# Kernel tuning notes

Hardware: AMD Instinct MI355X
Metric: run time of the kernel (lower is better)

Reference implementation:

```python
import jax, jax.numpy as jnp
import numpy as np
from jax import lax

V, E, Q, D = 100000, 300, 64, 4096
K = 5
NEG_SLOPE = 0.01


def setup_inputs() -> dict:
    key = jax.random.key(0)
    ks = jax.random.split(key, 16)
    return {
        "question": jax.random.randint(ks[0], (Q,), 0, V),
        "doc1": jax.random.randint(ks[1], (D,), 0, V),
        "doc2": jax.random.randint(ks[2], (D,), 0, V),
        "doc1_sim": jax.random.uniform(ks[3], (D, Q), dtype=jnp.float32),
        "doc2_sim": jax.random.uniform(ks[4], (D, Q), dtype=jnp.float32),
        "gaf": jax.random.normal(ks[5], (4,), dtype=jnp.float32),
        "baf": jax.random.normal(ks[6], (4,), dtype=jnp.float32),
        "emb": jax.random.normal(ks[7], (V, E), dtype=jnp.float32) * 0.1,
        "idf": jax.random.uniform(ks[8], (V, 1), dtype=jnp.float32) * 10.0,
        "conv_w": jax.random.normal(ks[9], (E, E, 3), dtype=jnp.float32) * (1.0 / np.sqrt(3 * E)),
        "conv_b": jax.random.normal(ks[10], (E,), dtype=jnp.float32) * 0.01,
        "qw_w": jax.random.normal(ks[11], (1, E + 1), dtype=jnp.float32) * (1.0 / np.sqrt(E + 1)),
        "qw_b": jax.random.normal(ks[12], (1,), dtype=jnp.float32) * 0.01,
        "lin1_w": jax.random.normal(ks[13], (8, 6), dtype=jnp.float32) * (1.0 / np.sqrt(6)),
        "lin2_w": jax.random.normal(ks[14], (1, 8), dtype=jnp.float32) * (1.0 / np.sqrt(8)),
        "out_w": jax.random.normal(ks[15], (1, 5), dtype=jnp.float32) * (1.0 / np.sqrt(5)),
    }


def _leaky(x):
    return jnp.where(x >= 0, x, NEG_SLOPE * x)


def _conv_residual(x, w, b):
    # x: [L, E]. Torch Conv1d(E,E,3,padding=2) followed by slice [1:L+1] is a
    # centered SAME conv; activation applied before the residual add.
    y = lax.conv_general_dilated(x.T[None], w, (1,), [(1, 1)],
                                 dimension_numbers=("NCW", "OIW", "NCW"))
    y = y[0] + b[:, None]            # [E, L]
    return _leaky(y).T + x           # [L, E]


def _cosine(A, B):
    # A: [Q, E], B: [L, E] -> [Q, L]
    num = A @ B.T
    den = jnp.linalg.norm(A, axis=-1)[:, None] * jnp.linalg.norm(B, axis=-1)[None, :]
    return num / den


def _kmax_pool(sim):
    # sim: [Q, L] -> [Q, 2] = (max, mean of top-K)
    top = lax.top_k(sim, K)[0]       # descending [Q, K]
    return jnp.stack([top[:, 0], jnp.mean(top, axis=-1)], axis=-1)


def _get_output(pooled_list, q_weights, lin1_w, lin2_w):
    temp = jnp.concatenate(pooled_list, axis=-1)     # [Q, 6]
    lo = _leaky(temp @ lin1_w.T) @ lin2_w.T          # [Q, 1]
    lo = lo[:, 0] * q_weights
    return jnp.sum(lo) / lo.shape[0]


def reference(question, doc1, doc2, doc1_sim, doc2_sim, gaf, baf,
              emb, idf, conv_w, conv_b, qw_w, qw_b, lin1_w, lin2_w, out_w):
    q_emb = emb[question]            # [Q, E]
    d1_emb = emb[doc1]               # [D, E]
    d2_emb = emb[doc2]

    sim_ins_d1 = _cosine(q_emb, d1_emb)
    sim_ins_d2 = _cosine(q_emb, d2_emb)

    q_conv = _conv_residual(q_emb, conv_w, conv_b)
    d1_conv = _conv_residual(d1_emb, conv_w, conv_b)
    d2_conv = _conv_residual(d2_emb, conv_w, conv_b)

    sim_sen_d1 = _cosine(q_conv, d1_conv)
    sim_sen_d2 = _cosine(q_conv, d2_conv)

    sim_oh_d1 = doc1_sim.T           # [Q, D]
    sim_oh_d2 = doc2_sim.T

    p_oh_d1, p_ins_d1, p_sen_d1 = _kmax_pool(sim_oh_d1), _kmax_pool(sim_ins_d1), _kmax_pool(sim_sen_d1)
    p_oh_d2, p_ins_d2, p_sen_d2 = _kmax_pool(sim_oh_d2), _kmax_pool(sim_ins_d2), _kmax_pool(sim_sen_d2)

    q_idfs = idf[question]           # [Q, 1]
    qw = jnp.concatenate([q_conv, q_idfs], axis=-1) @ qw_w.T + qw_b  # [Q, 1]
    q_weights = jax.nn.softmax(qw[:, 0], axis=-1)

    doc1_emit = _get_output([p_oh_d1, p_ins_d1, p_sen_d1], q_weights, lin1_w, lin2_w)
    doc2_emit = _get_output([p_oh_d2, p_ins_d2, p_sen_d2], q_weights, lin1_w, lin2_w)

    good_feats = jnp.concatenate([gaf, doc1_emit[None]])  # [5]
    bad_feats = jnp.concatenate([baf, doc2_emit[None]])
    good_out = out_w @ good_feats                          # [1]
    bad_out = out_w @ bad_feats

    loss1 = jnp.mean(jnp.maximum(0.0, -(good_out - bad_out) + 1.0))
    return (loss1, good_out, bad_out, loss1, loss1)
```

## Files before the change

### kernel.cpp

```cpp
#include <hip/hip_runtime.h>
#include <math.h>

#define EE 300
#define KP 320
#define LDSW 328
#define QQ 64
#define DD 4096
#define NEG 0.01f

typedef __attribute__((ext_vector_type(8))) short short8;
typedef __attribute__((ext_vector_type(4))) float f32x4;
typedef unsigned short ushort_t;

__device__ inline ushort_t f2bf(float f) {
  unsigned u = __builtin_bit_cast(unsigned, f);
  u += 0x7fff + ((u >> 16) & 1);
  return (ushort_t)(u >> 16);
}
__device__ inline float bf2f(ushort_t h) {
  return __builtin_bit_cast(float, (unsigned)h << 16);
}

#define GATHER_ROWS (66 + 4098 + 4098)
#define GATHER_BLOCKS ((GATHER_ROWS + 3) / 4)
#define WT_BLOCKS 143
#define TR_BLOCKS 128
#define ZERO_BLOCKS 9
#define PREP_BLOCKS (GATHER_BLOCKS + WT_BLOCKS + TR_BLOCKS + ZERO_BLOCKS)

__global__ __launch_bounds__(256) void prep(
    const float* __restrict__ emb, const int* __restrict__ question,
    const int* __restrict__ doc1, const int* __restrict__ doc2,
    const float* __restrict__ conv_w,
    const float* __restrict__ doc1_sim, const float* __restrict__ doc2_sim,
    ushort_t* __restrict__ qbe, ushort_t* __restrict__ d1be, ushort_t* __restrict__ d2be,
    ushort_t* __restrict__ qbc, ushort_t* __restrict__ d1bc, ushort_t* __restrict__ d2bc,
    ushort_t* __restrict__ wt2,
    float* __restrict__ ohT1, float* __restrict__ ohT2,
    float* __restrict__ nq2, float* __restrict__ nd12, float* __restrict__ nd22,
    float* __restrict__ acc_zero_base) {
  __shared__ float tilebuf[64][65];
  int b = blockIdx.x;
  int tid = threadIdx.x;
  if (b < GATHER_BLOCKS) {
    int w = tid >> 6, lane = tid & 63;
    int g = b * 4 + w;
    int t, row;
    if (g < 66)             { t = 0; row = g; }
    else if (g < 66 + 4098) { t = 1; row = g - 66; }
    else if (g < GATHER_ROWS) { t = 2; row = g - 66 - 4098; }
    else return;
    const int* idx = t == 0 ? question : (t == 1 ? doc1 : doc2);
    int L = t == 0 ? QQ : DD;
    ushort_t* be = t == 0 ? qbe : (t == 1 ? d1be : d2be);
    ushort_t* bc = t == 0 ? qbc : (t == 1 ? d1bc : d2bc);
    float* nrm2 = t == 0 ? nq2 : (t == 1 ? nd12 : nd22);
    if (row == 0 || row == L + 1) {
      for (int i = lane; i < KP; i += 64) be[(size_t)row * KP + i] = 0;
      return;
    }
    int r = row - 1;
    const float* src = emb + (size_t)idx[r] * EE;
    float ss = 0.f;
    for (int i = lane; i < EE; i += 64) {
      float v = src[i];
      be[(size_t)row * KP + i] = f2bf(v);
      ss += v * v;
    }
    for (int i = EE + lane; i < KP; i += 64) {
      be[(size_t)row * KP + i] = 0;
      bc[(size_t)r * KP + i] = 0;
    }
    #pragma unroll
    for (int o = 32; o; o >>= 1) ss += __shfl_xor(ss, o);
    if (lane == 0) nrm2[r] = ss;
  } else if (b < GATHER_BLOCKS + WT_BLOCKS) {
    int f = (b - GATHER_BLOCKS) * 4 + (tid >> 6);
    if (f >= 570) return;
    int lane = tid & 63;
    int ks = f % 10, n = (f / 10) % 19, tap = f / 190;
    int o = n * 16 + (lane & 15);
    int kbase = ks * 32 + (lane >> 4) * 8;
    ushort_t* dst = wt2 + (size_t)f * 512 + lane * 8;
    #pragma unroll
    for (int e = 0; e < 8; ++e) {
      int k = kbase + e;
      float v = (o < EE && k < EE) ? conv_w[((size_t)o * EE + k) * 3 + tap] : 0.f;
      dst[e] = f2bf(v);
    }
  } else if (b < GATHER_BLOCKS + WT_BLOCKS + TR_BLOCKS) {
    int idx = b - (GATHER_BLOCKS + WT_BLOCKS);
    int srcsel = idx >> 6, tile = idx & 63;
    const float* in = srcsel ? doc2_sim : doc1_sim;
    float* outT = srcsel ? ohT2 : ohT1;
    int c = tid & 63, rq = tid >> 6;
    #pragma unroll 4
    for (int i = 0; i < 16; ++i) {
      int r = i * 4 + rq;
      tilebuf[r][c] = in[(size_t)(tile * 64 + r) * QQ + c];
    }
    __syncthreads();
    #pragma unroll 4
    for (int i = 0; i < 16; ++i) {
      int q = i * 4 + rq;
      outT[(size_t)q * DD + tile * 64 + c] = tilebuf[c][q];
    }
  } else {
    int i0 = (b - (GATHER_BLOCKS + WT_BLOCKS + TR_BLOCKS)) * 1024 + tid;
    #pragma unroll
    for (int j = 0; j < 4; ++j) {
      int i = i0 + j * 256;
      if (i < 8320) acc_zero_base[i] = 0.f;
    }
  }
}

__global__ __launch_bounds__(256) void conv_mfma(
    const ushort_t* __restrict__ wt2, const float* __restrict__ bias,
    const float* __restrict__ qw_w,
    const ushort_t* __restrict__ qbe, const ushort_t* __restrict__ d1be,
    const ushort_t* __restrict__ d2be,
    ushort_t* __restrict__ qbc, ushort_t* __restrict__ d1bc,
    ushort_t* __restrict__ d2bc,
    float* __restrict__ nqc2, float* __restrict__ nd1c2, float* __restrict__ nd2c2,
    float* __restrict__ qwacc) {
  __shared__ ushort_t lds[34 * LDSW];
  int bx = blockIdx.x;
  int t, m0, yh;
  if (bx < 4) { t = 0; m0 = (bx >> 1) * 32; yh = bx & 1; }
  else {
    int i = bx - 4;
    t = 1 + (i >> 8);
    int j = i & 255;
    m0 = (j >> 1) * 32; yh = j & 1;
  }
  const ushort_t* be = t == 0 ? qbe : (t == 1 ? d1be : d2be);
  ushort_t* bc = t == 0 ? qbc : (t == 1 ? d1bc : d2bc);
  float* nc2 = t == 0 ? nqc2 : (t == 1 ? nd1c2 : nd2c2);
  int tid = threadIdx.x;
  for (int s = tid; s < 34 * 40; s += 256) {
    int row = s / 40, col = s - row * 40;
    *(short8*)(&lds[row * LDSW + col * 8]) =
        *(const short8*)(be + (size_t)(m0 + row) * KP + col * 8);
  }
  __syncthreads();
  int w = tid >> 6, lane = tid & 63, mrow = lane & 15, g = lane >> 4;
  int nstart, ncnt;
  if (yh == 0) { nstart = (w < 2) ? 3 * w : 2 * w + 2; ncnt = (w < 2) ? 3 : 2; }
  else         { nstart = (w == 0) ? 10 : 2 * w + 11;  ncnt = (w == 0) ? 3 : 2; }
  f32x4 acc[3][2];
  #pragma unroll
  for (int j = 0; j < 3; ++j)
    #pragma unroll
    for (int h = 0; h < 2; ++h) acc[j][h] = (f32x4){0.f, 0.f, 0.f, 0.f};

  for (int tap = 0; tap < 3; ++tap) {
    const ushort_t* alo = &lds[(mrow + tap) * LDSW + g * 8];
    #pragma unroll
    for (int ks = 0; ks < 10; ++ks) {
      short8 a0 = *(const short8*)(alo + ks * 32);
      short8 a1 = *(const short8*)(alo + 16 * LDSW + ks * 32);
      #pragma unroll
      for (int j = 0; j < 3; ++j) {
        if (j < ncnt) {
          short8 bfr = *(const short8*)(wt2 +
              (size_t)((tap * 19 + nstart + j) * 10 + ks) * 512 + lane * 8);
          acc[j][0] = __builtin_amdgcn_mfma_f32_16x16x32_bf16(a0, bfr, acc[j][0], 0, 0, 0);
          acc[j][1] = __builtin_amdgcn_mfma_f32_16x16x32_bf16(a1, bfr, acc[j][1], 0, 0, 0);
        }
      }
    }
  }
  float ss[2][4] = {{0.f,0.f,0.f,0.f},{0.f,0.f,0.f,0.f}};
  float yq[2][4] = {{0.f,0.f,0.f,0.f},{0.f,0.f,0.f,0.f}};
  #pragma unroll
  for (int j = 0; j < 3; ++j) {
    if (j < ncnt) {
      int col = (nstart + j) * 16 + mrow;
      if (col < EE) {
        float bcol = bias[col];
        float qwc = (t == 0) ? qw_w[col] : 0.f;
        #pragma unroll
        for (int h = 0; h < 2; ++h) {
          #pragma unroll
          for (int r = 0; r < 4; ++r) {
            int lrow = h * 16 + g * 4 + r;
            float y = acc[j][h][r] + bcol;
            y = (y >= 0.f) ? y : NEG * y;
            y += bf2f(lds[(1 + lrow) * LDSW + col]);
            bc[(size_t)(m0 + lrow) * KP + col] = f2bf(y);
            ss[h][r] += y * y;
            if (t == 0) yq[h][r] += y * qwc;
          }
        }
      }
    }
  }
  #pragma unroll
  for (int h = 0; h < 2; ++h) {
    #pragma unroll
    for (int r = 0; r < 4; ++r) {
      float s = ss[h][r];
      s += __shfl_xor(s, 1); s += __shfl_xor(s, 2);
      s += __shfl_xor(s, 4); s += __shfl_xor(s, 8);
      if (mrow == 0) atomicAdd(&nc2[m0 + h * 16 + g * 4 + r], s);
      if (t == 0) {
        float sq = yq[h][r];
        sq += __shfl_xor(sq, 1); sq += __shfl_xor(sq, 2);
        sq += __shfl_xor(sq, 4); sq += __shfl_xor(sq, 8);
        if (mrow == 0) atomicAdd(&qwacc[m0 + h * 16 + g * 4 + r], sq);
      }
    }
  }
}

__global__ __launch_bounds__(256) void sim_mfma(
    const ushort_t* __restrict__ qbe, const ushort_t* __restrict__ d1be,
    const ushort_t* __restrict__ d2be,
    const ushort_t* __restrict__ qbc, const ushort_t* __restrict__ d1bc,
    const ushort_t* __restrict__ d2bc,
    const float* __restrict__ nq2, const float* __restrict__ nd12,
    const float* __restrict__ nd22, const float* __restrict__ nqc2,
    const float* __restrict__ nd1c2, const float* __restrict__ nd2c2,
    float* __restrict__ sims) {
  __shared__ ushort_t lds[32 * LDSW];
  int s = blockIdx.y;
  const ushort_t* A = (s < 2) ? qbe + KP : qbc;
  const ushort_t* B = s == 0 ? d1be + KP : s == 1 ? d2be + KP : s == 2 ? d1bc : d2bc;
  const float* na2 = (s < 2) ? nq2 : nqc2;
  const float* nb2 = s == 0 ? nd12 : s == 1 ? nd22 : s == 2 ? nd1c2 : nd2c2;
  float* out = sims + (size_t)s * QQ * DD;
  int l0 = blockIdx.x * 32;
  int tid = threadIdx.x;
  for (int i = tid; i < 32 * 40; i += 256) {
    int row = i / 40, col = i - row * 40;
    *(short8*)(&lds[row * LDSW + col * 8]) =
        *(const short8*)(B + (size_t)(l0 + row) * KP + col * 8);
  }
  __syncthreads();
  int w = tid >> 6, lane = tid & 63, mrow = lane & 15, g = lane >> 4;
  f32x4 acc[2];
  acc[0] = (f32x4){0.f, 0.f, 0.f, 0.f};
  acc[1] = (f32x4){0.f, 0.f, 0.f, 0.f};
  const ushort_t* arow = A + (size_t)(w * 16 + mrow) * KP + g * 8;
  #pragma unroll
  for (int ks = 0; ks < 10; ++ks) {
    short8 a = *(const short8*)(arow + ks * 32);
    #pragma unroll
    for (int n = 0; n < 2; ++n) {
      short8 bfr = *(const short8*)(&lds[(n * 16 + mrow) * LDSW + g * 8 + ks * 32]);
      acc[n] = __builtin_amdgcn_mfma_f32_16x16x32_bf16(a, bfr, acc[n], 0, 0, 0);
    }
  }
  #pragma unroll
  for (int n = 0; n < 2; ++n) {
    int l = l0 + n * 16 + mrow;
    float inb = rsqrtf(nb2[l]);
    #pragma unroll
    for (int r = 0; r < 4; ++r) {
      int q = w * 16 + g * 4 + r;
      out[(size_t)q * DD + l] = acc[n][r] * rsqrtf(na2[q]) * inb;
    }
  }
}

__device__ inline void top5_insert(float* t, float v) {
  if (v > t[4]) {
    t[4] = v;
    #pragma unroll
    for (int j = 4; j > 0; --j) {
      if (t[j] > t[j - 1]) { float tmp = t[j]; t[j] = t[j - 1]; t[j - 1] = tmp; }
    }
  }
}

__global__ __launch_bounds__(256) void kmax_pool(
    const float* __restrict__ ohT1, const float* __restrict__ ohT2,
    const float* __restrict__ sims, float* __restrict__ pool) {
  int q = blockIdx.x, src = blockIdx.y;
  int tid = threadIdx.x;
  const size_t QD = (size_t)QQ * DD;
  const float* base;
  switch (src) {
    case 0: base = ohT1; break;
    case 1: base = sims + 0 * QD; break;
    case 2: base = sims + 2 * QD; break;
    case 3: base = ohT2; break;
    case 4: base = sims + 1 * QD; break;
    default: base = sims + 3 * QD; break;
  }
  const float* row = base + (size_t)q * DD;
  float t5[5];
  #pragma unroll
  for (int j = 0; j < 5; ++j) t5[j] = -1e30f;
  for (int l = tid; l < DD; l += 256) top5_insert(t5, row[l]);
  __shared__ float ls[256][5];
  #pragma unroll
  for (int j = 0; j < 5; ++j) ls[tid][j] = t5[j];
  __syncthreads();
  for (int step = 128; step >= 1; step >>= 1) {
    if (tid < step) {
      float a[5], c[5], m[5];
      #pragma unroll
      for (int j = 0; j < 5; ++j) { a[j] = ls[tid][j]; c[j] = ls[tid + step][j]; }
      int ia = 0, ib = 0;
      #pragma unroll
      for (int j = 0; j < 5; ++j) m[j] = (a[ia] >= c[ib]) ? a[ia++] : c[ib++];
      #pragma unroll
      for (int j = 0; j < 5; ++j) ls[tid][j] = m[j];
    }
    __syncthreads();
  }
  if (tid == 0) {
    float mx = ls[0][0];
    float sm = 0.f;
    #pragma unroll
    for (int j = 0; j < 5; ++j) sm += ls[0][j];
    pool[((size_t)src * QQ + q) * 2 + 0] = mx;
    pool[((size_t)src * QQ + q) * 2 + 1] = sm * 0.2f;
  }
}

__global__ void final_kernel(
    const float* __restrict__ qwacc, const float* __restrict__ idf,
    const int* __restrict__ question, const float* __restrict__ qw_w,
    const float* __restrict__ qw_b, const float* __restrict__ pool,
    const float* __restrict__ lin1_w, const float* __restrict__ lin2_w,
    const float* __restrict__ out_w, const float* __restrict__ gaf,
    const float* __restrict__ baf, float* __restrict__ out5) {
  int q = threadIdx.x;
  float s = qwacc[q] + qw_b[0] + idf[question[q]] * qw_w[EE];
  float m = s;
  #pragma unroll
  for (int o = 32; o; o >>= 1) m = fmaxf(m, __shfl_xor(m, o));
  float e = expf(s - m);
  float se = e;
  #pragma unroll
  for (int o = 32; o; o >>= 1) se += __shfl_xor(se, o);
  float qwgt = e / se;

  float emit[2];
  for (int doc = 0; doc < 2; ++doc) {
    float temp[6];
    #pragma unroll
    for (int j = 0; j < 3; ++j) {
      temp[2 * j]     = pool[(((size_t)doc * 3 + j) * QQ + q) * 2 + 0];
      temp[2 * j + 1] = pool[(((size_t)doc * 3 + j) * QQ + q) * 2 + 1];
    }
    float lo = 0.f;
    #pragma unroll
    for (int r = 0; r < 8; ++r) {
      float h = 0.f;
      #pragma unroll
      for (int c = 0; c < 6; ++c) h += lin1_w[r * 6 + c] * temp[c];
      h = (h >= 0.f) ? h : NEG * h;
      lo += lin2_w[r] * h;
    }
    lo *= qwgt;
    #pragma unroll
    for (int o = 32; o; o >>= 1) lo += __shfl_xor(lo, o);
    emit[doc] = lo / (float)QQ;
  }
  if (q == 0) {
    float good = out_w[0] * gaf[0] + out_w[1] * gaf[1] + out_w[2] * gaf[2] +
                 out_w[3] * gaf[3] + out_w[4] * emit[0];
    float bad  = out_w[0] * baf[0] + out_w[1] * baf[1] + out_w[2] * baf[2] +
                 out_w[3] * baf[3] + out_w[4] * emit[1];
    float l1 = fmaxf(0.f, -(good - bad) + 1.f);
    out5[0] = l1; out5[1] = good; out5[2] = bad; out5[3] = l1; out5[4] = l1;
  }
}

extern "C" void kernel_launch(void* const* d_in, const int* in_sizes, int n_in,
                              void* d_out, int out_size, void* d_ws, size_t ws_size,
                              hipStream_t stream) {
  (void)in_sizes; (void)n_in; (void)out_size; (void)ws_size;
  const int* question   = (const int*)d_in[0];
  const int* doc1       = (const int*)d_in[1];
  const int* doc2       = (const int*)d_in[2];
  const float* doc1_sim = (const float*)d_in[3];
  const float* doc2_sim = (const float*)d_in[4];
  const float* gaf      = (const float*)d_in[5];
  const float* baf      = (const float*)d_in[6];
  const float* emb      = (const float*)d_in[7];
  const float* idf      = (const float*)d_in[8];
  const float* conv_w   = (const float*)d_in[9];
  const float* conv_b   = (const float*)d_in[10];
  const float* qw_w     = (const float*)d_in[11];
  const float* qw_b     = (const float*)d_in[12];
  const float* lin1_w   = (const float*)d_in[13];
  const float* lin2_w   = (const float*)d_in[14];
  const float* out_w    = (const float*)d_in[15];
  float* out = (float*)d_out;

  char* p = (char*)d_ws;
  ushort_t* qbe  = (ushort_t*)p; p += (size_t)(QQ + 2) * KP * 2;
  ushort_t* d1be = (ushort_t*)p; p += (size_t)(DD + 2) * KP * 2;
  ushort_t* d2be = (ushort_t*)p; p += (size_t)(DD + 2) * KP * 2;
  ushort_t* qbc  = (ushort_t*)p; p += (size_t)QQ * KP * 2;
  ushort_t* d1bc = (ushort_t*)p; p += (size_t)DD * KP * 2;
  ushort_t* d2bc = (ushort_t*)p; p += (size_t)DD * KP * 2;
  ushort_t* wt2  = (ushort_t*)p; p += (size_t)570 * 512 * 2;
  float* sims = (float*)p; p += (size_t)4 * QQ * DD * 4;
  float* ohT1 = (float*)p; p += (size_t)QQ * DD * 4;
  float* ohT2 = (float*)p; p += (size_t)QQ * DD * 4;
  float* nq2  = (float*)p; p += QQ * 4;
  float* nd12 = (float*)p; p += DD * 4;
  float* nd22 = (float*)p; p += DD * 4;
  float* nqc2  = (float*)p; p += QQ * 4;
  float* nd1c2 = (float*)p; p += DD * 4;
  float* nd2c2 = (float*)p; p += DD * 4;
  float* qwacc = (float*)p; p += QQ * 4;
  float* pool  = (float*)p; p += 6 * QQ * 2 * 4;

  prep<<<PREP_BLOCKS, 256, 0, stream>>>(
      emb, question, doc1, doc2, conv_w, doc1_sim, doc2_sim,
      qbe, d1be, d2be, qbc, d1bc, d2bc, wt2, ohT1, ohT2,
      nq2, nd12, nd22, nqc2);

  conv_mfma<<<516, 256, 0, stream>>>(
      wt2, conv_b, qw_w, qbe, d1be, d2be, qbc, d1bc, d2bc,
      nqc2, nd1c2, nd2c2, qwacc);

  sim_mfma<<<dim3(DD / 32, 4), 256, 0, stream>>>(
      qbe, d1be, d2be, qbc, d1bc, d2bc,
      nq2, nd12, nd22, nqc2, nd1c2, nd2c2, sims);

  kmax_pool<<<dim3(QQ, 6), 256, 0, stream>>>(ohT1, ohT2, sims, pool);

  final_kernel<<<1, 64, 0, stream>>>(qwacc, idf, question, qw_w, qw_b, pool,
                                     lin1_w, lin2_w, out_w, gaf, baf, out);
}
```

Baseline: 62.10 us.

## Fuse similarity GEMM, top-k pooling and final head into one kernel

```diff
diff --git a/kernel.cpp b/kernel.cpp
--- a/kernel.cpp
+++ b/kernel.cpp
@@ -20,36 +20,40 @@
 __device__ inline float bf2f(ushort_t h) {
   return __builtin_bit_cast(float, (unsigned)h << 16);
 }
+__device__ inline void top5_insert(float* t, float v) {
+  if (v > t[4]) {
+    t[4] = v;
+    #pragma unroll
+    for (int j = 4; j > 0; --j)
+      if (t[j] > t[j - 1]) { float tmp = t[j]; t[j] = t[j - 1]; t[j - 1] = tmp; }
+  }
+}
 
 #define GATHER_ROWS (66 + 4098 + 4098)
 #define GATHER_BLOCKS ((GATHER_ROWS + 3) / 4)
 #define WT_BLOCKS 143
-#define TR_BLOCKS 128
 #define ZERO_BLOCKS 9
-#define PREP_BLOCKS (GATHER_BLOCKS + WT_BLOCKS + TR_BLOCKS + ZERO_BLOCKS)
+#define PREP_BLOCKS (GATHER_BLOCKS + WT_BLOCKS + ZERO_BLOCKS)
 
 __global__ __launch_bounds__(256) void prep(
     const float* __restrict__ emb, const int* __restrict__ question,
     const int* __restrict__ doc1, const int* __restrict__ doc2,
     const float* __restrict__ conv_w,
-    const float* __restrict__ doc1_sim, const float* __restrict__ doc2_sim,
     ushort_t* __restrict__ qbe, ushort_t* __restrict__ d1be, ushort_t* __restrict__ d2be,
     ushort_t* __restrict__ qbc, ushort_t* __restrict__ d1bc, ushort_t* __restrict__ d2bc,
     ushort_t* __restrict__ wt2,
-    float* __restrict__ ohT1, float* __restrict__ ohT2,
     float* __restrict__ nq2, float* __restrict__ nd12, float* __restrict__ nd22,
-    float* __restrict__ acc_zero_base) {
-  __shared__ float tilebuf[64][65];
+    float* __restrict__ zero_base, unsigned* __restrict__ cnts) {
   int b = blockIdx.x;
   int tid = threadIdx.x;
+  int wv = tid >> 6, lane = tid & 63;
   if (b < GATHER_BLOCKS) {
-    int w = tid >> 6, lane = tid & 63;
-    int g = b * 4 + w;
+    int g = b * 4 + wv;
+    if (g >= GATHER_ROWS) return;
     int t, row;
     if (g < 66)             { t = 0; row = g; }
     else if (g < 66 + 4098) { t = 1; row = g - 66; }
-    else if (g < GATHER_ROWS) { t = 2; row = g - 66 - 4098; }
-    else return;
+    else                    { t = 2; row = g - 4164; }
     const int* idx = t == 0 ? question : (t == 1 ? doc1 : doc2);
     int L = t == 0 ? QQ : DD;
     ushort_t* be = t == 0 ? qbe : (t == 1 ? d1be : d2be);
@@ -75,9 +79,8 @@
     for (int o = 32; o; o >>= 1) ss += __shfl_xor(ss, o);
     if (lane == 0) nrm2[r] = ss;
   } else if (b < GATHER_BLOCKS + WT_BLOCKS) {
-    int f = (b - GATHER_BLOCKS) * 4 + (tid >> 6);
+    int f = (b - GATHER_BLOCKS) * 4 + wv;
     if (f >= 570) return;
-    int lane = tid & 63;
     int ks = f % 10, n = (f / 10) % 19, tap = f / 190;
     int o = n * 16 + (lane & 15);
     int kbase = ks * 32 + (lane >> 4) * 8;
@@ -88,29 +91,14 @@
       float v = (o < EE && k < EE) ? conv_w[((size_t)o * EE + k) * 3 + tap] : 0.f;
       dst[e] = f2bf(v);
     }
-  } else if (b < GATHER_BLOCKS + WT_BLOCKS + TR_BLOCKS) {
-    int idx = b - (GATHER_BLOCKS + WT_BLOCKS);
-    int srcsel = idx >> 6, tile = idx & 63;
-    const float* in = srcsel ? doc2_sim : doc1_sim;
-    float* outT = srcsel ? ohT2 : ohT1;
-    int c = tid & 63, rq = tid >> 6;
-    #pragma unroll 4
-    for (int i = 0; i < 16; ++i) {
-      int r = i * 4 + rq;
-      tilebuf[r][c] = in[(size_t)(tile * 64 + r) * QQ + c];
-    }
-    __syncthreads();
-    #pragma unroll 4
-    for (int i = 0; i < 16; ++i) {
-      int q = i * 4 + rq;
-      outT[(size_t)q * DD + tile * 64 + c] = tilebuf[c][q];
-    }
   } else {
-    int i0 = (b - (GATHER_BLOCKS + WT_BLOCKS + TR_BLOCKS)) * 1024 + tid;
+    int zb = b - (GATHER_BLOCKS + WT_BLOCKS);
+    if (zb == 0 && tid < 8) cnts[tid] = 0u;
+    int i0 = zb * 1024 + tid;
     #pragma unroll
     for (int j = 0; j < 4; ++j) {
       int i = i0 + j * 256;
-      if (i < 8320) acc_zero_base[i] = 0.f;
+      if (i < 8320) zero_base[i] = 0.f;
     }
   }
 }
@@ -144,10 +132,10 @@
         *(const short8*)(be + (size_t)(m0 + row) * KP + col * 8);
   }
   __syncthreads();
-  int w = tid >> 6, lane = tid & 63, mrow = lane & 15, g = lane >> 4;
+  int wv = tid >> 6, lane = tid & 63, mrow = lane & 15, g = lane >> 4;
   int nstart, ncnt;
-  if (yh == 0) { nstart = (w < 2) ? 3 * w : 2 * w + 2; ncnt = (w < 2) ? 3 : 2; }
-  else         { nstart = (w == 0) ? 10 : 2 * w + 11;  ncnt = (w == 0) ? 3 : 2; }
+  if (yh == 0) { nstart = (wv < 2) ? 3 * wv : 2 * wv + 2; ncnt = (wv < 2) ? 3 : 2; }
+  else         { nstart = (wv == 0) ? 10 : 2 * wv + 11;   ncnt = (wv == 0) ? 3 : 2; }
   f32x4 acc[3][2];
   #pragma unroll
   for (int j = 0; j < 3; ++j)
@@ -214,7 +202,7 @@
   }
 }
 
-__global__ __launch_bounds__(256) void sim_mfma(
+__global__ __launch_bounds__(256) void simpoolfinal(
     const ushort_t* __restrict__ qbe, const ushort_t* __restrict__ d1be,
     const ushort_t* __restrict__ d2be,
     const ushort_t* __restrict__ qbc, const ushort_t* __restrict__ d1bc,
@@ -222,152 +210,165 @@
     const float* __restrict__ nq2, const float* __restrict__ nd12,
     const float* __restrict__ nd22, const float* __restrict__ nqc2,
     const float* __restrict__ nd1c2, const float* __restrict__ nd2c2,
-    float* __restrict__ sims) {
-  __shared__ ushort_t lds[32 * LDSW];
-  int s = blockIdx.y;
-  const ushort_t* A = (s < 2) ? qbe + KP : qbc;
-  const ushort_t* B = s == 0 ? d1be + KP : s == 1 ? d2be + KP : s == 2 ? d1bc : d2bc;
-  const float* na2 = (s < 2) ? nq2 : nqc2;
-  const float* nb2 = s == 0 ? nd12 : s == 1 ? nd22 : s == 2 ? nd1c2 : nd2c2;
-  float* out = sims + (size_t)s * QQ * DD;
-  int l0 = blockIdx.x * 32;
-  int tid = threadIdx.x;
-  for (int i = tid; i < 32 * 40; i += 256) {
-    int row = i / 40, col = i - row * 40;
-    *(short8*)(&lds[row * LDSW + col * 8]) =
-        *(const short8*)(B + (size_t)(l0 + row) * KP + col * 8);
-  }
-  __syncthreads();
-  int w = tid >> 6, lane = tid & 63, mrow = lane & 15, g = lane >> 4;
-  f32x4 acc[2];
-  acc[0] = (f32x4){0.f, 0.f, 0.f, 0.f};
-  acc[1] = (f32x4){0.f, 0.f, 0.f, 0.f};
-  const ushort_t* arow = A + (size_t)(w * 16 + mrow) * KP + g * 8;
-  #pragma unroll
-  for (int ks = 0; ks < 10; ++ks) {
-    short8 a = *(const short8*)(arow + ks * 32);
-    #pragma unroll
-    for (int n = 0; n < 2; ++n) {
-      short8 bfr = *(const short8*)(&lds[(n * 16 + mrow) * LDSW + g * 8 + ks * 32]);
-      acc[n] = __builtin_amdgcn_mfma_f32_16x16x32_bf16(a, bfr, acc[n], 0, 0, 0);
-    }
-  }
-  #pragma unroll
-  for (int n = 0; n < 2; ++n) {
-    int l = l0 + n * 16 + mrow;
-    float inb = rsqrtf(nb2[l]);
-    #pragma unroll
-    for (int r = 0; r < 4; ++r) {
-      int q = w * 16 + g * 4 + r;
-      out[(size_t)q * DD + l] = acc[n][r] * rsqrtf(na2[q]) * inb;
-    }
-  }
-}
-
-__device__ inline void top5_insert(float* t, float v) {
-  if (v > t[4]) {
-    t[4] = v;
-    #pragma unroll
-    for (int j = 4; j > 0; --j) {
-      if (t[j] > t[j - 1]) { float tmp = t[j]; t[j] = t[j - 1]; t[j - 1] = tmp; }
-    }
-  }
-}
-
-__global__ __launch_bounds__(256) void kmax_pool(
-    const float* __restrict__ ohT1, const float* __restrict__ ohT2,
-    const float* __restrict__ sims, float* __restrict__ pool) {
-  int q = blockIdx.x, src = blockIdx.y;
-  int tid = threadIdx.x;
-  const size_t QD = (size_t)QQ * DD;
-  const float* base;
-  switch (src) {
-    case 0: base = ohT1; break;
-    case 1: base = sims + 0 * QD; break;
-    case 2: base = sims + 2 * QD; break;
-    case 3: base = ohT2; break;
-    case 4: base = sims + 1 * QD; break;
-    default: base = sims + 3 * QD; break;
-  }
-  const float* row = base + (size_t)q * DD;
-  float t5[5];
-  #pragma unroll
-  for (int j = 0; j < 5; ++j) t5[j] = -1e30f;
-  for (int l = tid; l < DD; l += 256) top5_insert(t5, row[l]);
-  __shared__ float ls[256][5];
-  #pragma unroll
-  for (int j = 0; j < 5; ++j) ls[tid][j] = t5[j];
-  __syncthreads();
-  for (int step = 128; step >= 1; step >>= 1) {
-    if (tid < step) {
-      float a[5], c[5], m[5];
-      #pragma unroll
-      for (int j = 0; j < 5; ++j) { a[j] = ls[tid][j]; c[j] = ls[tid + step][j]; }
-      int ia = 0, ib = 0;
-      #pragma unroll
-      for (int j = 0; j < 5; ++j) m[j] = (a[ia] >= c[ib]) ? a[ia++] : c[ib++];
-      #pragma unroll
-      for (int j = 0; j < 5; ++j) ls[tid][j] = m[j];
-    }
-    __syncthreads();
-  }
-  if (tid == 0) {
-    float mx = ls[0][0];
-    float sm = 0.f;
-    #pragma unroll
-    for (int j = 0; j < 5; ++j) sm += ls[0][j];
-    pool[((size_t)src * QQ + q) * 2 + 0] = mx;
-    pool[((size_t)src * QQ + q) * 2 + 1] = sm * 0.2f;
-  }
-}
-
-__global__ void final_kernel(
+    const float* __restrict__ d1sim, const float* __restrict__ d2sim,
+    float* __restrict__ pt5, unsigned* __restrict__ cnts, float* __restrict__ pool,
     const float* __restrict__ qwacc, const float* __restrict__ idf,
     const int* __restrict__ question, const float* __restrict__ qw_w,
-    const float* __restrict__ qw_b, const float* __restrict__ pool,
-    const float* __restrict__ lin1_w, const float* __restrict__ lin2_w,
-    const float* __restrict__ out_w, const float* __restrict__ gaf,
-    const float* __restrict__ baf, float* __restrict__ out5) {
-  int q = threadIdx.x;
-  float s = qwacc[q] + qw_b[0] + idf[question[q]] * qw_w[EE];
-  float m = s;
-  #pragma unroll
-  for (int o = 32; o; o >>= 1) m = fmaxf(m, __shfl_xor(m, o));
-  float e = expf(s - m);
-  float se = e;
-  #pragma unroll
-  for (int o = 32; o; o >>= 1) se += __shfl_xor(se, o);
-  float qwgt = e / se;
-
-  float emit[2];
-  for (int doc = 0; doc < 2; ++doc) {
-    float temp[6];
-    #pragma unroll
-    for (int j = 0; j < 3; ++j) {
-      temp[2 * j]     = pool[(((size_t)doc * 3 + j) * QQ + q) * 2 + 0];
-      temp[2 * j + 1] = pool[(((size_t)doc * 3 + j) * QQ + q) * 2 + 1];
-    }
-    float lo = 0.f;
-    #pragma unroll
-    for (int r = 0; r < 8; ++r) {
-      float h = 0.f;
-      #pragma unroll
-      for (int c = 0; c < 6; ++c) h += lin1_w[r * 6 + c] * temp[c];
-      h = (h >= 0.f) ? h : NEG * h;
-      lo += lin2_w[r] * h;
-    }
-    lo *= qwgt;
-    #pragma unroll
-    for (int o = 32; o; o >>= 1) lo += __shfl_xor(lo, o);
-    emit[doc] = lo / (float)QQ;
-  }
-  if (q == 0) {
-    float good = out_w[0] * gaf[0] + out_w[1] * gaf[1] + out_w[2] * gaf[2] +
-                 out_w[3] * gaf[3] + out_w[4] * emit[0];
-    float bad  = out_w[0] * baf[0] + out_w[1] * baf[1] + out_w[2] * baf[2] +
-                 out_w[3] * baf[3] + out_w[4] * emit[1];
-    float l1 = fmaxf(0.f, -(good - bad) + 1.f);
-    out5[0] = l1; out5[1] = good; out5[2] = bad; out5[3] = l1; out5[4] = l1;
+    const float* __restrict__ qw_b, const float* __restrict__ lin1_w,
+    const float* __restrict__ lin2_w, const float* __restrict__ out_w,
+    const float* __restrict__ gaf, const float* __restrict__ baf,
+    float* __restrict__ out5) {
+  __shared__ ushort_t ldsB[32 * LDSW];
+  __shared__ float strip[64][33];
+  __shared__ unsigned oldv;
+  int task = blockIdx.x;
+  int tid = threadIdx.x;
+  int wv = tid >> 6, lane = tid & 63;
+  int ps, chunk;
+
+  if (task < 512) {
+    int s = task >> 7;
+    chunk = task & 127;
+    ps = (s == 0) ? 1 : (s == 1) ? 4 : (s == 2) ? 2 : 5;
+    int l0 = chunk * 32;
+    const ushort_t* A = (s < 2) ? qbe + KP : qbc;
+    const ushort_t* B = s == 0 ? d1be + KP : s == 1 ? d2be + KP
+                      : s == 2 ? d1bc : d2bc;
+    const float* na2 = (s < 2) ? nq2 : nqc2;
+    const float* nb2 = s == 0 ? nd12 : s == 1 ? nd22 : s == 2 ? nd1c2 : nd2c2;
+    for (int i = tid; i < 32 * 40; i += 256) {
+      int row = i / 40, col = i - row * 40;
+      *(short8*)(&ldsB[row * LDSW + col * 8]) =
+          *(const short8*)(B + (size_t)(l0 + row) * KP + col * 8);
+    }
+    __syncthreads();
+    int mrow = lane & 15, g = lane >> 4;
+    f32x4 acc[2];
+    acc[0] = (f32x4){0.f, 0.f, 0.f, 0.f};
+    acc[1] = (f32x4){0.f, 0.f, 0.f, 0.f};
+    const ushort_t* arow = A + (size_t)(wv * 16 + mrow) * KP + g * 8;
+    #pragma unroll
+    for (int ks = 0; ks < 10; ++ks) {
+      short8 a = *(const short8*)(arow + ks * 32);
+      #pragma unroll
+      for (int n = 0; n < 2; ++n) {
+        short8 bfr = *(const short8*)(&ldsB[(n * 16 + mrow) * LDSW + g * 8 + ks * 32]);
+        acc[n] = __builtin_amdgcn_mfma_f32_16x16x32_bf16(a, bfr, acc[n], 0, 0, 0);
+      }
+    }
+    #pragma unroll
+    for (int n = 0; n < 2; ++n) {
+      int l = n * 16 + mrow;
+      float inb = rsqrtf(nb2[l0 + l]);
+      #pragma unroll
+      for (int r = 0; r < 4; ++r) {
+        int q = wv * 16 + g * 4 + r;
+        strip[q][l] = acc[n][r] * rsqrtf(na2[q]) * inb;
+      }
+    }
+  } else {
+    int o = (task - 512) >> 7;
+    chunk = task & 127;
+    ps = o ? 3 : 0;
+    const float* dsim = o ? d2sim : d1sim;
+    int l0 = chunk * 32;
+    int r = tid >> 3, q0 = (tid & 7) * 8;
+    const float* srcp = dsim + (size_t)(l0 + r) * QQ + q0;
+    f32x4 v0 = *(const f32x4*)srcp;
+    f32x4 v1 = *(const f32x4*)(srcp + 4);
+    #pragma unroll
+    for (int e = 0; e < 4; ++e) strip[q0 + e][r] = v0[e];
+    #pragma unroll
+    for (int e = 0; e < 4; ++e) strip[q0 + 4 + e][r] = v1[e];
+  }
+  __syncthreads();
+
+  if (tid < 64) {
+    float t5[5] = {-1e30f, -1e30f, -1e30f, -1e30f, -1e30f};
+    #pragma unroll
+    for (int l = 0; l < 32; ++l) top5_insert(t5, strip[tid][l]);
+    float* dst = pt5 + (((size_t)ps * QQ + tid) * 128 + chunk) * 8;
+    *(f32x4*)dst = (f32x4){t5[0], t5[1], t5[2], t5[3]};
+    *(f32x4*)(dst + 4) = (f32x4){t5[4], -1e30f, -1e30f, -1e30f};
+  }
+  __threadfence();
+  __syncthreads();
+  if (tid == 0) oldv = atomicAdd(&cnts[ps], 1u);
+  __syncthreads();
+  if (oldv != 127u) return;
+
+  __threadfence();
+  for (int i = 0; i < 16; ++i) {
+    int q = wv * 16 + i;
+    const float* p0 = pt5 + (((size_t)ps * QQ + q) * 128 + 2 * lane) * 8;
+    float t5[5] = {-1e30f, -1e30f, -1e30f, -1e30f, -1e30f};
+    #pragma unroll
+    for (int c = 0; c < 2; ++c)
+      #pragma unroll
+      for (int j = 0; j < 5; ++j) top5_insert(t5, p0[c * 8 + j]);
+    #pragma unroll
+    for (int mask = 1; mask < 64; mask <<= 1) {
+      float a[5], bb[5];
+      #pragma unroll
+      for (int j = 0; j < 5; ++j) { a[j] = t5[j]; bb[j] = __shfl_xor(t5[j], mask); }
+      int ia = 0, ib = 0;
+      #pragma unroll
+      for (int j = 0; j < 5; ++j) t5[j] = (a[ia] >= bb[ib]) ? a[ia++] : bb[ib++];
+    }
+    if (lane == 0) {
+      float sm = t5[0] + t5[1] + t5[2] + t5[3] + t5[4];
+      pool[((size_t)ps * QQ + q) * 2 + 0] = t5[0];
+      pool[((size_t)ps * QQ + q) * 2 + 1] = sm * 0.2f;
+    }
+  }
+  __threadfence();
+  __syncthreads();
+  if (tid == 0) oldv = atomicAdd(&cnts[6], 1u);
+  __syncthreads();
+  if (oldv != 5u) return;
+
+  __threadfence();
+  if (tid < 64) {
+    int q = tid;
+    float s = qwacc[q] + qw_b[0] + idf[question[q]] * qw_w[EE];
+    float m = s;
+    #pragma unroll
+    for (int o = 32; o; o >>= 1) m = fmaxf(m, __shfl_xor(m, o));
+    float e = expf(s - m);
+    float se = e;
+    #pragma unroll
+    for (int o = 32; o; o >>= 1) se += __shfl_xor(se, o);
+    float qwgt = e / se;
+    float emit[2];
+    for (int doc = 0; doc < 2; ++doc) {
+      float temp[6];
+      #pragma unroll
+      for (int j = 0; j < 3; ++j) {
+        temp[2 * j]     = pool[(((size_t)doc * 3 + j) * QQ + q) * 2 + 0];
+        temp[2 * j + 1] = pool[(((size_t)doc * 3 + j) * QQ + q) * 2 + 1];
+      }
+      float lo = 0.f;
+      #pragma unroll
+      for (int r = 0; r < 8; ++r) {
+        float h = 0.f;
+        #pragma unroll
+        for (int c = 0; c < 6; ++c) h += lin1_w[r * 6 + c] * temp[c];
+        h = (h >= 0.f) ? h : NEG * h;
+        lo += lin2_w[r] * h;
+      }
+      lo *= qwgt;
+      #pragma unroll
+      for (int o = 32; o; o >>= 1) lo += __shfl_xor(lo, o);
+      emit[doc] = lo / (float)QQ;
+    }
+    if (q == 0) {
+      float good = out_w[0] * gaf[0] + out_w[1] * gaf[1] + out_w[2] * gaf[2] +
+                   out_w[3] * gaf[3] + out_w[4] * emit[0];
+      float bad  = out_w[0] * baf[0] + out_w[1] * baf[1] + out_w[2] * baf[2] +
+                   out_w[3] * baf[3] + out_w[4] * emit[1];
+      float l1 = fmaxf(0.f, -(good - bad) + 1.f);
+      out5[0] = l1; out5[1] = good; out5[2] = bad; out5[3] = l1; out5[4] = l1;
+    }
   }
 }
 
@@ -401,33 +402,29 @@
   ushort_t* d1bc = (ushort_t*)p; p += (size_t)DD * KP * 2;
   ushort_t* d2bc = (ushort_t*)p; p += (size_t)DD * KP * 2;
   ushort_t* wt2  = (ushort_t*)p; p += (size_t)570 * 512 * 2;
-  float* sims = (float*)p; p += (size_t)4 * QQ * DD * 4;
-  float* ohT1 = (float*)p; p += (size_t)QQ * DD * 4;
-  float* ohT2 = (float*)p; p += (size_t)QQ * DD * 4;
-  float* nq2  = (float*)p; p += QQ * 4;
-  float* nd12 = (float*)p; p += DD * 4;
-  float* nd22 = (float*)p; p += DD * 4;
+  float* nq2   = (float*)p; p += QQ * 4;
+  float* nd12  = (float*)p; p += DD * 4;
+  float* nd22  = (float*)p; p += DD * 4;
   float* nqc2  = (float*)p; p += QQ * 4;
   float* nd1c2 = (float*)p; p += DD * 4;
   float* nd2c2 = (float*)p; p += DD * 4;
   float* qwacc = (float*)p; p += QQ * 4;
+  float* pt5   = (float*)p; p += (size_t)6 * QQ * 128 * 8 * 4;
   float* pool  = (float*)p; p += 6 * QQ * 2 * 4;
+  unsigned* cnts = (unsigned*)p; p += 8 * 4;
 
   prep<<<PREP_BLOCKS, 256, 0, stream>>>(
-      emb, question, doc1, doc2, conv_w, doc1_sim, doc2_sim,
-      qbe, d1be, d2be, qbc, d1bc, d2bc, wt2, ohT1, ohT2,
-      nq2, nd12, nd22, nqc2);
+      emb, question, doc1, doc2, conv_w,
+      qbe, d1be, d2be, qbc, d1bc, d2bc, wt2,
+      nq2, nd12, nd22, nqc2, cnts);
 
   conv_mfma<<<516, 256, 0, stream>>>(
       wt2, conv_b, qw_w, qbe, d1be, d2be, qbc, d1bc, d2bc,
       nqc2, nd1c2, nd2c2, qwacc);
 
-  sim_mfma<<<dim3(DD / 32, 4), 256, 0, stream>>>(
+  simpoolfinal<<<768, 256, 0, stream>>>(
       qbe, d1be, d2be, qbc, d1bc, d2bc,
-      nq2, nd12, nd22, nqc2, nd1c2, nd2c2, sims);
-
-  kmax_pool<<<dim3(QQ, 6), 256, 0, stream>>>(ohT1, ohT2, sims, pool);
-
-  final_kernel<<<1, 64, 0, stream>>>(qwacc, idf, question, qw_w, qw_b, pool,
-                                     lin1_w, lin2_w, out_w, gaf, baf, out);
-}
+      nq2, nd12, nd22, nqc2, nd1c2, nd2c2,
+      doc1_sim, doc2_sim, pt5, cnts, pool,
+      qwacc, idf, question, qw_w, qw_b, lin1_w, lin2_w, out_w, gaf, baf, out);
+}
```

Result: slower. 195.7 us (+215.1%).
